# Optimization experiments

Measured on AMD Instinct MI355X. Metric: run time of the kernel, lower is better.

Reference implementation:

```python
import jax, jax.numpy as jnp
import numpy as np

NUM_TOKENS = 8192
HIDDEN = 4096
NUM_EXPERTS = 64
TOP_K = 8


def setup_inputs() -> dict:
    key = jax.random.key(0)
    k1, k2, k3 = jax.random.split(key, 3)
    tokens = jax.random.normal(k1, (NUM_TOKENS, HIDDEN), dtype=jnp.float32)
    token_probs = jax.random.uniform(k2, (NUM_TOKENS, NUM_EXPERTS), dtype=jnp.float32)
    # exactly TOP_K experts per token -> static num_out_tokens
    scores = jax.random.normal(k3, (NUM_TOKENS, NUM_EXPERTS))
    _, topk_idx = jax.lax.top_k(scores, TOP_K)  # [T, K]
    rows = jnp.arange(NUM_TOKENS)[:, None]
    routing_map = jnp.zeros((NUM_TOKENS, NUM_EXPERTS), dtype=bool).at[rows, topk_idx].set(True)
    return {
        "tokens": tokens,
        "token_probs": token_probs,
        "routing_map": routing_map,
        "num_out_tokens": NUM_TOKENS * TOP_K,
    }


def reference(tokens, token_probs, routing_map, num_out_tokens):
    # Fallback (non-fused) path of TurboTokenPermuter.forward.
    num_tokens, _ = tokens.shape
    # routing_map.bool().T -> [E, T]; masked_select in row-major order =
    # for each expert (in order), the token ids routed to it (in token order).
    flat_mask = routing_map.T.reshape(-1)  # [E*T]
    # stable argsort of ~mask puts flat positions of True entries first, in order
    perm = jnp.argsort(~flat_mask, stable=True)[:num_out_tokens]  # flat E*T indices
    sorted_indices = (perm % num_tokens).astype(jnp.int32)  # token ids (column index)
    permuted_probs = token_probs.T.reshape(-1)[perm]
    permuted_input = tokens[sorted_indices]  # index_select along dim 0
    return permuted_input, permuted_probs, sorted_indices
```

## Files before the change

kernel.cpp:

```cpp
#include <hip/hip_runtime.h>
#include <stdint.h>

#define NTOK   8192
#define NEXP   64
#define HID    4096
#define TOPK   8
#define OUTROW 65536
#define CHUNK  256
#define NCHUNK 32
#define NPART  2048

typedef float f32x4 __attribute__((ext_vector_type(4)));
typedef unsigned long long u64;

__global__ void mask_count_kernel(const int* __restrict__ map,
                                  u64* __restrict__ masks,
                                  int* __restrict__ pcnt) {
    int b = blockIdx.x;
    int e = b >> 5, c = b & (NCHUNK - 1);
    int tid = threadIdx.x;
    int w = tid >> 6, lane = tid & 63;

    __shared__ u64 sm[CHUNK];
    int t0 = c * CHUNK + w * 64;
#pragma unroll 8
    for (int i = 0; i < 64; ++i) {
        int v = map[(size_t)(t0 + i) * NEXP + lane];
        u64 bal = __ballot(v != 0);
        if (lane == 0) sm[w * 64 + i] = bal;
    }
    __syncthreads();
    if (e == 0) masks[c * CHUNK + tid] = sm[tid];

    __shared__ int red[256];
    red[tid] = (int)((sm[tid] >> e) & 1ull);
    __syncthreads();
    for (int off = 128; off > 0; off >>= 1) {
        if (tid < off) red[tid] += red[tid + off];
        __syncthreads();
    }
    if (tid == 0) pcnt[b] = red[0];
}

__global__ void assign_kernel(const u64* __restrict__ masks,
                              const float* __restrict__ probs,
                              const int* __restrict__ pcnt,
                              int* __restrict__ tok_pos,
                              float* __restrict__ probs_out,
                              float* __restrict__ idx_out) {
    int b = blockIdx.x;
    int e = b >> 5, c = b & (NCHUNK - 1);
    int tid = threadIdx.x;
    int w = tid >> 6, lane = tid & 63;

    __shared__ int red[256];
    __shared__ int wcnt[4];

    int acc = 0;
    for (int i = tid; i < b; i += 256) acc += pcnt[i];
    red[tid] = acc;
    __syncthreads();
    for (int off = 128; off > 0; off >>= 1) {
        if (tid < off) red[tid] += red[tid + off];
        __syncthreads();
    }
    int base = red[0];

    int t = c * CHUNK + tid;
    u64 mk = masks[t];
    bool m = (mk >> e) & 1ull;
    u64 bal = __ballot(m);
    int rank = __popcll(bal & ((1ull << lane) - 1ull));
    if (lane == 0) wcnt[w] = __popcll(bal);
    __syncthreads();
    int wbase = 0;
#pragma unroll
    for (int i = 0; i < 4; ++i) wbase += (i < w) ? wcnt[i] : 0;

    if (m) {
        int pos = base + wbase + rank;
        idx_out[pos] = (float)t;
        probs_out[pos] = probs[(size_t)t * NEXP + e];
        int slot = __popcll(mk & ((1ull << e) - 1ull));
        if (slot < TOPK) tok_pos[t * TOPK + slot] = pos;
    }
}

__global__ void gather_kernel(const float* __restrict__ tokens,
                              const int* __restrict__ tok_pos,
                              float* __restrict__ out_rows) {
    int t = blockIdx.x;
    int tid = threadIdx.x;
    const f32x4* sp = (const f32x4*)(tokens + (size_t)t * HID);
    f32x4 v0 = sp[tid];
    f32x4 v1 = sp[tid + 256];
    f32x4 v2 = sp[tid + 512];
    f32x4 v3 = sp[tid + 768];
#pragma unroll
    for (int j = 0; j < TOPK; ++j) {
        unsigned p = (unsigned)tok_pos[t * TOPK + j];
        if (p >= OUTROW) continue;
        f32x4* dp = (f32x4*)(out_rows + (size_t)p * HID);
        dp[tid]       = v0;
        dp[tid + 256] = v1;
        dp[tid + 512] = v2;
        dp[tid + 768] = v3;
    }
}

extern "C" void kernel_launch(void* const* d_in, const int* in_sizes, int n_in,
                              void* d_out, int out_size, void* d_ws, size_t ws_size,
                              hipStream_t stream) {
    const float* tokens = (const float*)d_in[0];
    const float* probs  = (const float*)d_in[1];
    const int*   map    = (const int*)d_in[2];

    float* out_rows  = (float*)d_out;
    float* out_probs = out_rows + (size_t)OUTROW * HID;
    float* out_idx   = out_probs + OUTROW;

    u64* masks   = (u64*)d_ws;
    int* pcnt    = (int*)(masks + NTOK);
    int* tok_pos = pcnt + NPART;

    mask_count_kernel<<<NPART, 256, 0, stream>>>(map, masks, pcnt);
    assign_kernel<<<NPART, 256, 0, stream>>>(masks, probs, pcnt, tok_pos,
                                             out_probs, out_idx);
    gather_kernel<<<NTOK, 256, 0, stream>>>(tokens, tok_pos, out_rows);
}
```

Baseline: 277.8 us.

## Compute per-chunk expert histograms once per chunk and use nontemporal gather copies

The mask/count kernel previously ran one block per (expert, chunk) pair, so the 8 MB routing map was re-read by all 64 experts. It now runs one block per chunk, builds the bitmask once, and fills a 64-bin shared-memory histogram with atomics, writing counts in the same expert-major layout. The gather kernel also switches to nontemporal loads and stores for the large token copy, to reduce cache pollution. The trade-off is only 32 blocks in the mask kernel, which leaves most of the GPU idle during that stage.

```diff
diff --git a/kernel.cpp b/kernel.cpp
--- a/kernel.cpp
+++ b/kernel.cpp
@@ -16,12 +16,14 @@
 __global__ void mask_count_kernel(const int* __restrict__ map,
                                   u64* __restrict__ masks,
                                   int* __restrict__ pcnt) {
-    int b = blockIdx.x;
-    int e = b >> 5, c = b & (NCHUNK - 1);
+    int c = blockIdx.x;
     int tid = threadIdx.x;
     int w = tid >> 6, lane = tid & 63;
 
     __shared__ u64 sm[CHUNK];
+    __shared__ int hcnt[NEXP];
+    if (tid < NEXP) hcnt[tid] = 0;
+
     int t0 = c * CHUNK + w * 64;
 #pragma unroll 8
     for (int i = 0; i < 64; ++i) {
@@ -30,16 +32,16 @@
         if (lane == 0) sm[w * 64 + i] = bal;
     }
     __syncthreads();
-    if (e == 0) masks[c * CHUNK + tid] = sm[tid];
 
-    __shared__ int red[256];
-    red[tid] = (int)((sm[tid] >> e) & 1ull);
+    u64 mk = sm[tid];
+    masks[c * CHUNK + tid] = mk;
+    while (mk) {
+        int e = __ffsll((long long)mk) - 1;
+        atomicAdd(&hcnt[e], 1);
+        mk &= mk - 1;
+    }
     __syncthreads();
-    for (int off = 128; off > 0; off >>= 1) {
-        if (tid < off) red[tid] += red[tid + off];
-        __syncthreads();
-    }
-    if (tid == 0) pcnt[b] = red[0];
+    if (tid < NEXP) pcnt[tid * NCHUNK + c] = hcnt[tid];
 }
 
 __global__ void assign_kernel(const u64* __restrict__ masks,
@@ -92,19 +94,19 @@
     int t = blockIdx.x;
     int tid = threadIdx.x;
     const f32x4* sp = (const f32x4*)(tokens + (size_t)t * HID);
-    f32x4 v0 = sp[tid];
-    f32x4 v1 = sp[tid + 256];
-    f32x4 v2 = sp[tid + 512];
-    f32x4 v3 = sp[tid + 768];
+    f32x4 v0 = __builtin_nontemporal_load(sp + tid);
+    f32x4 v1 = __builtin_nontemporal_load(sp + tid + 256);
+    f32x4 v2 = __builtin_nontemporal_load(sp + tid + 512);
+    f32x4 v3 = __builtin_nontemporal_load(sp + tid + 768);
 #pragma unroll
     for (int j = 0; j < TOPK; ++j) {
         unsigned p = (unsigned)tok_pos[t * TOPK + j];
         if (p >= OUTROW) continue;
         f32x4* dp = (f32x4*)(out_rows + (size_t)p * HID);
-        dp[tid]       = v0;
-        dp[tid + 256] = v1;
-        dp[tid + 512] = v2;
-        dp[tid + 768] = v3;
+        __builtin_nontemporal_store(v0, dp + tid);
+        __builtin_nontemporal_store(v1, dp + tid + 256);
+        __builtin_nontemporal_store(v2, dp + tid + 512);
+        __builtin_nontemporal_store(v3, dp + tid + 768);
     }
 }
 
@@ -123,8 +125,8 @@
     int* pcnt    = (int*)(masks + NTOK);
     int* tok_pos = pcnt + NPART;
 
-    mask_count_kernel<<<NPART, 256, 0, stream>>>(map, masks, pcnt);
-    assign_kernel<<<NPART, 256, 0, stream>>>(masks, probs, pcnt, tok_pos,
-                                             out_probs, out_idx);
-    gather_kernel<<<NTOK, 256, 0, stream>>>(tokens, tok_pos, out_rows);
+    mask_count_kernel<<<NCHUNK, CHUNK, 0, stream>>>(map, masks, pcnt);
+    assign_kernel<<<NPART, CHUNK, 0, stream>>>(masks, probs, pcnt, tok_pos,
+                                               out_probs, out_idx);
+    gather_kernel<<<NTOK, CHUNK, 0, stream>>>(tokens, tok_pos, out_rows);
 }
```

New measurement: 271.4 us. 2.3% less time.
